# Performance work log

Measured on AMD Instinct MI355X. Metric: run time of the kernel, lower is better.

The kernel has to match this reference:

```python
import jax, jax.numpy as jnp
import numpy as np

N_IM, N_OBJ = 16, 16          # images, objects per image
D_IN = 2048                    # obj_pair_feat_dim
PER_IM = N_OBJ * (N_OBJ + 1) // 2   # obj boxes + union boxes per image
N_BOX = N_IM * PER_IM               # 2176
N_PAIR = N_IM * N_OBJ * (N_OBJ - 1) # is_ex=True -> 2*C(n,2) per image = 3840
NUM_REL = 3


def setup_inputs() -> dict:
    rng = np.random.default_rng(0)
    H, W = 600.0, 800.0
    boxes = np.zeros((N_BOX, 5), np.float32)
    o1i, o2i, ui, imi = [], [], [], []
    for i in range(N_IM):
        off = i * PER_IM
        x1 = rng.uniform(0, W / 2, N_OBJ); y1 = rng.uniform(0, H / 2, N_OBJ)
        bw = rng.uniform(10, W / 2, N_OBJ); bh = rng.uniform(10, H / 2, N_OBJ)
        boxes[off:off + N_OBJ] = np.stack([np.full(N_OBJ, i), x1, y1, x1 + bw, y1 + bh], 1)
        uc = off + N_OBJ
        for a in range(N_OBJ):
            for b in range(a + 1, N_OBJ):
                boxes[uc] = [i, min(x1[a], x1[b]), min(y1[a], y1[b]),
                             max(x1[a] + bw[a], x1[b] + bw[b]), max(y1[a] + bh[a], y1[b] + bh[b])]
                o1i += [off + a, off + b]; o2i += [off + b, off + a]
                ui += [uc, uc]; imi += [i, i]
                uc += 1
    im_info = np.tile(np.array([H, W, 1.0], np.float32), (N_IM, 1))
    key = jax.random.key(0)
    ks = jax.random.split(key, 16)
    lin = lambda k, i, o: jax.random.normal(k, (i, o), jnp.float32) * 0.02
    return dict(
        xs=jax.random.normal(ks[0], (N_PAIR, D_IN), jnp.float32) * 0.1,
        xo=jax.random.normal(ks[1], (N_PAIR, D_IN), jnp.float32) * 0.1,
        xu=jax.random.normal(ks[2], (N_PAIR, D_IN), jnp.float32) * 0.1,
        boxes=jnp.asarray(boxes), im_info=jnp.asarray(im_info),
        o1_idx=jnp.asarray(o1i, jnp.int32), o2_idx=jnp.asarray(o2i, jnp.int32),
        u_idx=jnp.asarray(ui, jnp.int32), img_idx=jnp.asarray(imi, jnp.int32),
        Ws1=lin(ks[3], D_IN, 512), bs1=jnp.zeros(512, jnp.float32),
        Ws2=lin(ks[4], 512, 256), bs2=jnp.zeros(256, jnp.float32),
        Wo1=lin(ks[5], D_IN, 512), bo1=jnp.zeros(512, jnp.float32),
        Wo2=lin(ks[6], 512, 256), bo2=jnp.zeros(256, jnp.float32),
        Wu1=lin(ks[7], D_IN, 512), bu1=jnp.zeros(512, jnp.float32),
        Wu2=lin(ks[8], 512, 256), bu2=jnp.zeros(256, jnp.float32),
        Wc1=lin(ks[9], 256 + 19, 256), bc1=jnp.zeros(256, jnp.float32),
        Wc2=lin(ks[10], 256, NUM_REL), bc2=jnp.zeros(NUM_REL, jnp.float32),
    )


def _mlp(x, W1, b1, W2, b2):
    return jax.nn.relu(jax.nn.relu(x @ W1 + b1) @ W2 + b2)


def _encode_loc(sb, ob, ub, hw):
    # sb/ob/ub: [P,4] (x1,y1,x2,y2); hw: [P,2] (h_i, w_i)
    h_i, w_i = hw[:, 0], hw[:, 1]
    x_s = (sb[:, 0] + sb[:, 2]) / 2.0; y_s = (sb[:, 1] + sb[:, 3]) / 2.0
    w_s = sb[:, 2] - sb[:, 0]; h_s = sb[:, 3] - sb[:, 1]
    x_o = (ob[:, 0] + ob[:, 2]) / 2.0; y_o = (ob[:, 1] + ob[:, 3]) / 2.0
    w_o = ob[:, 2] - ob[:, 0]; h_o = ob[:, 3] - ob[:, 1]
    a_s = w_s * h_s; a_o = w_o * h_o
    a_u = (ub[:, 2] - ub[:, 0]) * (ub[:, 3] - ub[:, 1])
    area = w_i * h_i
    return jnp.stack([
        x_s / w_i, y_s / h_i, (x_s + w_s) / w_i, (y_s + h_s) / h_i, a_s / area,
        x_o / w_i, y_o / h_i, (x_o + w_o) / w_i, (y_o + h_o) / h_i, a_o / area,
        (x_s - x_o) / w_o, (y_s - y_o) / h_o, jnp.log(w_s / w_o), jnp.log(h_s / h_o),
        (x_o - x_s) / w_s, (y_o - y_s) / h_s, jnp.log(w_o / w_s), jnp.log(h_o / h_s),
        a_u / area], axis=1)  # [P,19]


def reference(xs, xo, xu, boxes, im_info, o1_idx, o2_idx, u_idx, img_idx,
              Ws1, bs1, Ws2, bs2, Wo1, bo1, Wo2, bo2, Wu1, bu1, Wu2, bu2,
              Wc1, bc1, Wc2, bc2):
    fs = _mlp(xs, Ws1, bs1, Ws2, bs2)
    fo = _mlp(xo, Wo1, bo1, Wo2, bo2)
    fu = _mlp(xu, Wu1, bu1, Wu2, bu2)
    appear = fu - fo - fs                              # [P,256]
    loc = _encode_loc(boxes[o1_idx, 1:5], boxes[o2_idx, 1:5],
                      boxes[u_idx, 1:5], im_info[img_idx, :2])  # [P,19]
    h = jax.nn.relu(jnp.concatenate([appear, loc], axis=1) @ Wc1 + bc1)
    return h @ Wc2 + bc2                               # [P,num_rel]
```

## Files before the change

kernel.cpp:

```cpp
#include <hip/hip_runtime.h>

#define N_PAIR 3840

typedef short bf16x8 __attribute__((ext_vector_type(8)));
typedef float f32x4 __attribute__((ext_vector_type(4)));

static __device__ __forceinline__ ushort f2bf(float f) {
    uint x = __float_as_uint(f);
    uint r = (x + 0x7FFFu + ((x >> 16) & 1u)) >> 16;
    return (ushort)r;
}
static __device__ __forceinline__ float bf2f(ushort u) {
    return __uint_as_float(((uint)u) << 16);
}

#define GLOAD16(GP, LP)                                                        \
    __builtin_amdgcn_global_load_lds(                                          \
        (const __attribute__((address_space(1))) void*)(GP),                   \
        (__attribute__((address_space(3))) void*)(LP), 16, 0, 0)

static __device__ __forceinline__ bf16x8 cvt8(float4 lo, float4 hi4) {
    union { bf16x8 v; uint u[4]; } r;
    asm("v_cvt_pk_bf16_f32 %0, %1, %2" : "=v"(r.u[0]) : "v"(lo.x), "v"(lo.y));
    asm("v_cvt_pk_bf16_f32 %0, %1, %2" : "=v"(r.u[1]) : "v"(lo.z), "v"(lo.w));
    asm("v_cvt_pk_bf16_f32 %0, %1, %2" : "=v"(r.u[2]) : "v"(hi4.x), "v"(hi4.y));
    asm("v_cvt_pk_bf16_f32 %0, %1, %2" : "=v"(r.u[3]) : "v"(hi4.z), "v"(hi4.w));
    return r.v;
}

__global__ void transpose_convert(const float* __restrict__ in0,
                                  const float* __restrict__ in1,
                                  const float* __restrict__ in2,
                                  ushort* __restrict__ out,
                                  int K, int N, int Kpad) {
    const float* in = (blockIdx.z == 0) ? in0 : (blockIdx.z == 1 ? in1 : in2);
    ushort* o = out + (size_t)blockIdx.z * N * Kpad;
    __shared__ float tile[64][65];
    int k0 = blockIdx.x * 64, n0 = blockIdx.y * 64;
    int t = threadIdx.x;
    int r = t >> 2, c4 = (t & 3) * 16;
#pragma unroll
    for (int i = 0; i < 16; i++) {
        int k = k0 + r, n = n0 + c4 + i;
        tile[r][c4 + i] = (k < K && n < N) ? in[(size_t)k * N + n] : 0.f;
    }
    __syncthreads();
#pragma unroll
    for (int i = 0; i < 16; i++) {
        int n = n0 + r, k = k0 + c4 + i;
        if (n < N && k < Kpad) o[(size_t)n * Kpad + k] = f2bf(tile[c4 + i][r]);
    }
}

__global__ void transpose_convert2(const float* __restrict__ Ws2,
                                   const float* __restrict__ Wo2,
                                   const float* __restrict__ Wu2,
                                   const float* __restrict__ Wc1,
                                   ushort* __restrict__ W2T,
                                   ushort* __restrict__ WC1T) {
    int z = blockIdx.z;
    const float* in; ushort* o; int K, N, Kpad;
    if (z < 3) {
        in = (z == 0) ? Ws2 : (z == 1 ? Wo2 : Wu2);
        o = W2T + (size_t)z * 256 * 512; K = 512; N = 256; Kpad = 512;
    } else {
        in = Wc1; o = WC1T; K = 275; N = 256; Kpad = 288;
    }
    __shared__ float tile[64][65];
    int k0 = blockIdx.x * 64, n0 = blockIdx.y * 64;
    int t = threadIdx.x;
    int r = t >> 2, c4 = (t & 3) * 16;
#pragma unroll
    for (int i = 0; i < 16; i++) {
        int k = k0 + r, n = n0 + c4 + i;
        tile[r][c4 + i] = (k < K && n < N) ? in[(size_t)k * N + n] : 0.f;
    }
    __syncthreads();
#pragma unroll
    for (int i = 0; i < 16; i++) {
        int n = n0 + r, k = k0 + c4 + i;
        if (n < N && k < Kpad) o[(size_t)n * Kpad + k] = f2bf(tile[c4 + i][r]);
    }
}

__device__ __forceinline__ bf16x8 frag_ld(const ushort* __restrict__ lds, int row, int colbyte) {
    int off = (row << 7) + (colbyte ^ ((row & 7) << 4));
    return *reinterpret_cast<const bf16x8*>(reinterpret_cast<const char*>(lds) + off);
}
__device__ __forceinline__ bf16x8 frag32_ld(const ushort* __restrict__ lds, int row, int colbyte) {
    int off = (row << 6) + (colbyte ^ ((row & 3) << 4));
    return *reinterpret_cast<const bf16x8*>(reinterpret_cast<const char*>(lds) + off);
}

__global__ __launch_bounds__(256) void gemm1_main(const float* __restrict__ xs,
                                                  const float* __restrict__ xo,
                                                  const float* __restrict__ xu,
                                                  const ushort* __restrict__ w1t,
                                                  float* __restrict__ part) {
    int bid = blockIdx.x;
    int w = (bid & 7) * 90 + (bid >> 3);
    int br = w / 240; int r = w - br * 240;
    int mt = r >> 3, nt = (r >> 1) & 3, ks = r & 1;

    const float* x = br == 0 ? xs : (br == 1 ? xo : xu);
    const ushort* wt = w1t + (size_t)br * 512 * 2048;
    float* out = part + ((size_t)(ks * 3 + br)) * 3840 * 512;

    __shared__ float Af[128 * 64];
    __shared__ ushort Bs[128 * 64];
    int t = threadIdx.x, lane = t & 63, wid = t >> 6;
    int wr = wid >> 1, wc = wid & 1;
    int m0 = mt * 128, n0 = nt * 128, k0 = ks * 1024;
    const float* asrc = x + (size_t)m0 * 2048 + k0;
    const ushort* bsrc = wt + (size_t)n0 * 2048 + k0;
    int hi = lane >> 4, l15 = lane & 15;

    const float* aptr[8];
    const ushort* bptr[4];
#pragma unroll
    for (int i = 0; i < 8; i++) {
        int row = (wid * 8 + i) * 4 + (lane >> 4);
        int c16 = (lane & 15) ^ (row & 15);
        aptr[i] = asrc + (size_t)row * 2048 + (c16 << 2);
    }
#pragma unroll
    for (int i = 0; i < 4; i++) {
        int row = (wid * 4 + i) * 8 + (lane >> 3);
        int c8 = (lane & 7) ^ (row & 7);
        bptr[i] = bsrc + (size_t)row * 2048 + (c8 << 3);
    }

    f32x4 acc[4][4] = {};
#pragma unroll
    for (int i = 0; i < 8; i++) GLOAD16(aptr[i], &Af[((wid * 8 + i) * 64 + lane) * 4]);
#pragma unroll
    for (int i = 0; i < 4; i++) GLOAD16(bptr[i], &Bs[((wid * 4 + i) * 64 + lane) * 8]);
    __syncthreads();

    for (int kt = 0; kt < 1024; kt += 64) {
#pragma unroll
        for (int kk = 0; kk < 64; kk += 32) {
            int kf = kk + hi * 8;
            int c0 = kf >> 2;
            bf16x8 a[4], b[4];
#pragma unroll
            for (int i = 0; i < 4; i++) {
                int ra = wr * 64 + i * 16 + l15;
                const char* ab = reinterpret_cast<const char*>(&Af[0]);
                float4 lo = *reinterpret_cast<const float4*>(ab + ra * 256 + ((c0 ^ (ra & 15)) << 4));
                float4 h4 = *reinterpret_cast<const float4*>(ab + ra * 256 + (((c0 + 1) ^ (ra & 15)) << 4));
                a[i] = cvt8(lo, h4);
            }
#pragma unroll
            for (int j = 0; j < 4; j++)
                b[j] = frag_ld(&Bs[0], wc * 64 + j * 16 + l15, kf << 1);
#pragma unroll
            for (int i = 0; i < 4; i++)
#pragma unroll
                for (int j = 0; j < 4; j++)
                    acc[i][j] = __builtin_amdgcn_mfma_f32_16x16x32_bf16(a[i], b[j], acc[i][j], 0, 0, 0);
        }
        __syncthreads();
        if (kt + 64 < 1024) {
#pragma unroll
            for (int i = 0; i < 8; i++) GLOAD16(aptr[i] + kt + 64, &Af[((wid * 8 + i) * 64 + lane) * 4]);
#pragma unroll
            for (int i = 0; i < 4; i++) GLOAD16(bptr[i] + kt + 64, &Bs[((wid * 4 + i) * 64 + lane) * 8]);
            __syncthreads();
        }
    }
    int rb = m0 + wr * 64 + (hi << 2);
    int cb0 = n0 + wc * 64 + l15;
#pragma unroll
    for (int j = 0; j < 4; j++) {
        int col = cb0 + j * 16;
#pragma unroll
        for (int i = 0; i < 4; i++)
#pragma unroll
            for (int q = 0; q < 4; q++)
                out[(size_t)(rb + i * 16 + q) * 512 + col] = acc[i][j][q];
    }
}

__global__ void reduce_h1(const float* __restrict__ part,
                          const float* __restrict__ bs1,
                          const float* __restrict__ bo1,
                          const float* __restrict__ bu1,
                          ushort* __restrict__ h1) {
    const size_t D = (size_t)3840 * 512;
    size_t e = ((size_t)blockIdx.x * 256 + threadIdx.x) * 8;
    if (e >= 3 * D) return;
    int br = (int)(e / D);
    int col = (int)(e & 511);
    const float* bias = br == 0 ? bs1 : (br == 1 ? bo1 : bu1);
    const float4* p0 = reinterpret_cast<const float4*>(part + e);
    const float4* p1 = reinterpret_cast<const float4*>(part + 3 * D + e);
    const float4* bp = reinterpret_cast<const float4*>(bias + col);
    float4 a0 = p0[0], a1 = p0[1];
    float4 b0 = p1[0], b1 = p1[1];
    float4 c0 = bp[0], c1 = bp[1];
    union { bf16x8 v; ushort us[8]; } r;
#pragma unroll
    for (int i = 0; i < 4; i++) {
        float v = a0[i] + b0[i] + c0[i];
        r.us[i] = f2bf(v > 0.f ? v : 0.f);
        float w = a1[i] + b1[i] + c1[i];
        r.us[4 + i] = f2bf(w > 0.f ? w : 0.f);
    }
    *reinterpret_cast<bf16x8*>(h1 + e) = r.v;
}

__global__ __launch_bounds__(256) void gemm2(const ushort* __restrict__ h1,
                                             const ushort* __restrict__ w2t,
                                             const float* __restrict__ b_s,
                                             const float* __restrict__ b_o,
                                             const float* __restrict__ b_u,
                                             ushort* __restrict__ h2br) {
    int bid = blockIdx.x;
    int w = (bid & 7) * 45 + (bid >> 3);
    int br = w / 120; int r = w - br * 120;
    int xt = r >> 1, yt = r & 1;

    const ushort* A = h1 + (size_t)br * 3840 * 512;
    const ushort* B = w2t + (size_t)br * 256 * 512;
    const float* bias = br == 0 ? b_s : (br == 1 ? b_o : b_u);
    ushort* out = h2br + (size_t)br * 3840 * 256;

    __shared__ ushort As[2][64 * 64];
    __shared__ ushort Bs[2][128 * 64];
    int t = threadIdx.x, lane = t & 63, wid = t >> 6;
    int wr = wid >> 1, wc = wid & 1;
    int m0 = xt * 64, n0 = yt * 128;
    const ushort* asrc = A + (size_t)m0 * 512;
    const ushort* bsrc = B + (size_t)n0 * 512;

#define G2_GLOADS(BUF, KT)                                                                \
    {                                                                                     \
        _Pragma("unroll")                                                                 \
        for (int it = 0; it < 2; it++) {                                                  \
            int g = (wid * 2 + it) * 64 + lane;                                           \
            int rr = g >> 3, cc = g & 7;                                                  \
            const ushort* gp = asrc + (size_t)rr * 512 + (KT) + ((cc ^ (rr & 7)) << 3);   \
            GLOAD16(gp, &As[BUF][g * 8]);                                                 \
        }                                                                                 \
        _Pragma("unroll")                                                                 \
        for (int it = 0; it < 4; it++) {                                                  \
            int g = (wid * 4 + it) * 64 + lane;                                           \
            int rr = g >> 3, cc = g & 7;                                                  \
            const ushort* gp = bsrc + (size_t)rr * 512 + (KT) + ((cc ^ (rr & 7)) << 3);   \
            GLOAD16(gp, &Bs[BUF][g * 8]);                                                 \
        }                                                                                 \
    }
#define G2_MFMA(BUF)                                                                      \
    _Pragma("unroll")                                                                     \
    for (int kk = 0; kk < 64; kk += 32) {                                                 \
        int cb = (kk + ((lane >> 4) << 3)) << 1;                                          \
        bf16x8 a[2], b[4];                                                                \
        _Pragma("unroll")                                                                 \
        for (int i = 0; i < 2; i++) a[i] = frag_ld(&As[BUF][0], wr * 32 + i * 16 + (lane & 15), cb); \
        _Pragma("unroll")                                                                 \
        for (int f = 0; f < 4; f++) b[f] = frag_ld(&Bs[BUF][0], wc * 64 + f * 16 + (lane & 15), cb); \
        _Pragma("unroll")                                                                 \
        for (int i = 0; i < 2; i++)                                                       \
            _Pragma("unroll")                                                             \
            for (int j = 0; j < 4; j++)                                                   \
                acc[i][j] = __builtin_amdgcn_mfma_f32_16x16x32_bf16(a[i], b[j], acc[i][j], 0, 0, 0); \
    }

    f32x4 acc[2][4] = {};
    G2_GLOADS(0, 0)
    __syncthreads();
    int cur = 0;
    for (int kt = 0; kt < 512; kt += 64) {
        if (kt + 64 < 512) G2_GLOADS(cur ^ 1, kt + 64)
        G2_MFMA(cur)
        __syncthreads();
        cur ^= 1;
    }
    int rb = m0 + wr * 32 + ((lane >> 4) << 2);
    int cb0 = n0 + wc * 64 + (lane & 15);
#pragma unroll
    for (int j = 0; j < 4; j++) {
        int col = cb0 + j * 16;
        float bv = bias[col];
#pragma unroll
        for (int i = 0; i < 2; i++)
#pragma unroll
            for (int q = 0; q < 4; q++) {
                int row = rb + i * 16 + q;
                float v = acc[i][j][q] + bv;
                v = v > 0.f ? v : 0.f;
                out[(size_t)row * 256 + col] = f2bf(v);
            }
    }
#undef G2_GLOADS
#undef G2_MFMA
}

__global__ void appear_pack(const ushort* __restrict__ h2br,
                            ushort* __restrict__ hin,
                            const float* __restrict__ boxes,
                            const float* __restrict__ im_info,
                            const int* __restrict__ o1, const int* __restrict__ o2,
                            const int* __restrict__ u, const int* __restrict__ im) {
    int i = blockIdx.x * 256 + threadIdx.x;
    if (i < N_PAIR * 32) {
        int p = i >> 5, ch = (i & 31) * 8;
        const ushort* ps = h2br + (size_t)p * 256 + ch;
        bf16x8 vs = *reinterpret_cast<const bf16x8*>(ps);
        bf16x8 vo = *reinterpret_cast<const bf16x8*>(ps + (size_t)3840 * 256);
        bf16x8 vu = *reinterpret_cast<const bf16x8*>(ps + (size_t)2 * 3840 * 256);
        union { bf16x8 v; ushort us[8]; } r;
#pragma unroll
        for (int j = 0; j < 8; j++)
            r.us[j] = f2bf(bf2f(((ushort)vu[j])) - bf2f(((ushort)vo[j])) - bf2f(((ushort)vs[j])));
        *reinterpret_cast<bf16x8*>(hin + (size_t)p * 288 + ch) = r.v;
    }
    if (blockIdx.x < 15) {
        int p = blockIdx.x * 256 + threadIdx.x;
        const float* sb = boxes + 5 * o1[p] + 1;
        const float* ob = boxes + 5 * o2[p] + 1;
        const float* ub = boxes + 5 * u[p] + 1;
        const float* ii = im_info + 3 * im[p];
        float hi = ii[0], wi = ii[1];
        float x_s = (sb[0] + sb[2]) * 0.5f, y_s = (sb[1] + sb[3]) * 0.5f;
        float w_s = sb[2] - sb[0], h_s = sb[3] - sb[1];
        float x_o = (ob[0] + ob[2]) * 0.5f, y_o = (ob[1] + ob[3]) * 0.5f;
        float w_o = ob[2] - ob[0], h_o = ob[3] - ob[1];
        float a_s = w_s * h_s, a_o = w_o * h_o;
        float a_u = (ub[2] - ub[0]) * (ub[3] - ub[1]);
        float area = wi * hi;
        float f[19];
        f[0] = x_s / wi;            f[1] = y_s / hi;
        f[2] = (x_s + w_s) / wi;    f[3] = (y_s + h_s) / hi;
        f[4] = a_s / area;
        f[5] = x_o / wi;            f[6] = y_o / hi;
        f[7] = (x_o + w_o) / wi;    f[8] = (y_o + h_o) / hi;
        f[9] = a_o / area;
        f[10] = (x_s - x_o) / w_o;  f[11] = (y_s - y_o) / h_o;
        f[12] = logf(w_s / w_o);    f[13] = logf(h_s / h_o);
        f[14] = (x_o - x_s) / w_s;  f[15] = (y_o - y_s) / h_s;
        f[16] = logf(w_o / w_s);    f[17] = logf(h_o / h_s);
        f[18] = a_u / area;
        ushort* row = hin + (size_t)p * 288 + 256;
#pragma unroll
        for (int k = 0; k < 19; k++) row[k] = f2bf(f[k]);
#pragma unroll
        for (int k = 19; k < 32; k++) row[k] = 0;
    }
}

__global__ __launch_bounds__(256) void gemm3(const ushort* __restrict__ hin,
                                             const ushort* __restrict__ wc1t,
                                             const float* __restrict__ bc1,
                                             ushort* __restrict__ h2) {
    __shared__ ushort As[2][64 * 32];
    __shared__ ushort Bs[2][128 * 32];
    int t = threadIdx.x, lane = t & 63, wid = t >> 6;
    int wr = wid >> 1, wc = wid & 1;
    int m0 = blockIdx.x * 64, n0 = blockIdx.y * 128;
    const ushort* asrc = hin + (size_t)m0 * 288;
    const ushort* bsrc = wc1t + (size_t)n0 * 288;

    int ar = t >> 2, ac = (t & 3) * 8;
    bf16x8 pa, pb[2];
    auto issue = [&](int kt) {
        pa = *reinterpret_cast<const bf16x8*>(asrc + (size_t)ar * 288 + kt + ac);
#pragma unroll
        for (int it = 0; it < 2; it++) {
            int e = (it * 256 + t) * 8;
            int rr = e >> 5, cc = e & 31;
            pb[it] = *reinterpret_cast<const bf16x8*>(bsrc + (size_t)rr * 288 + kt + cc);
        }
    };
    auto commit = [&](int buf) {
        char* ab = reinterpret_cast<char*>(&As[buf][0]);
        int off0 = (ar << 6) + ((ac << 1) ^ ((ar & 3) << 4));
        *reinterpret_cast<bf16x8*>(ab + off0) = pa;
        char* bb = reinterpret_cast<char*>(&Bs[buf][0]);
#pragma unroll
        for (int it = 0; it < 2; it++) {
            int e = (it * 256 + t) * 8;
            int rr = e >> 5, cc = e & 31;
            int off = (rr << 6) + ((cc << 1) ^ ((rr & 3) << 4));
            *reinterpret_cast<bf16x8*>(bb + off) = pb[it];
        }
    };

    f32x4 acc[2][4] = {};
    issue(0);
    commit(0);
    __syncthreads();
    int cur = 0;
    for (int kt = 0; kt < 288; kt += 32) {
        int nxt = kt + 32;
        if (nxt < 288) issue(nxt);
        int cb = ((lane >> 4) << 3) << 1;
        bf16x8 a[2], b[4];
#pragma unroll
        for (int i = 0; i < 2; i++) a[i] = frag32_ld(&As[cur][0], wr * 32 + i * 16 + (lane & 15), cb);
#pragma unroll
        for (int f = 0; f < 4; f++) b[f] = frag32_ld(&Bs[cur][0], wc * 64 + f * 16 + (lane & 15), cb);
#pragma unroll
        for (int i = 0; i < 2; i++)
#pragma unroll
            for (int j = 0; j < 4; j++)
                acc[i][j] = __builtin_amdgcn_mfma_f32_16x16x32_bf16(a[i], b[j], acc[i][j], 0, 0, 0);
        if (nxt < 288) commit(cur ^ 1);
        __syncthreads();
        cur ^= 1;
    }
    int rb = m0 + wr * 32 + ((lane >> 4) << 2);
    int cb0 = n0 + wc * 64 + (lane & 15);
#pragma unroll
    for (int j = 0; j < 4; j++) {
        int col = cb0 + j * 16;
        float bv = bc1[col];
#pragma unroll
        for (int i = 0; i < 2; i++)
#pragma unroll
            for (int q = 0; q < 4; q++) {
                int row = rb + i * 16 + q;
                float v = acc[i][j][q] + bv;
                v = v > 0.f ? v : 0.f;
                h2[(size_t)row * 256 + col] = f2bf(v);
            }
    }
}

__global__ void final_fc(const ushort* __restrict__ h2,
                         const float* __restrict__ wc2,
                         const float* __restrict__ bc2,
                         float* __restrict__ out) {
    __shared__ float w[768];
    int t = threadIdx.x;
    for (int i = t; i < 768; i += 256) w[i] = wc2[i];
    __syncthreads();
    int g = t >> 4, l = t & 15;
    int row = blockIdx.x * 16 + g;
    const ushort* hr = h2 + (size_t)row * 256 + l * 16;
    bf16x8 v0 = *reinterpret_cast<const bf16x8*>(hr);
    bf16x8 v1 = *reinterpret_cast<const bf16x8*>(hr + 8);
    float s0 = 0.f, s1 = 0.f, s2 = 0.f;
#pragma unroll
    for (int k = 0; k < 8; k++) {
        float h = bf2f((ushort)v0[k]);
        int c = (l * 16 + k) * 3;
        s0 += h * w[c]; s1 += h * w[c + 1]; s2 += h * w[c + 2];
    }
#pragma unroll
    for (int k = 0; k < 8; k++) {
        float h = bf2f((ushort)v1[k]);
        int c = (l * 16 + 8 + k) * 3;
        s0 += h * w[c]; s1 += h * w[c + 1]; s2 += h * w[c + 2];
    }
#pragma unroll
    for (int m = 1; m < 16; m <<= 1) {
        s0 += __shfl_xor(s0, m);
        s1 += __shfl_xor(s1, m);
        s2 += __shfl_xor(s2, m);
    }
    if (l == 0) {
        out[row * 3 + 0] = s0 + bc2[0];
        out[row * 3 + 1] = s1 + bc2[1];
        out[row * 3 + 2] = s2 + bc2[2];
    }
}

extern "C" void kernel_launch(void* const* d_in, const int* in_sizes, int n_in,
                              void* d_out, int out_size, void* d_ws, size_t ws_size,
                              hipStream_t stream) {
    (void)in_sizes; (void)n_in; (void)out_size; (void)ws_size;
    const float* xs = (const float*)d_in[0];
    const float* xo = (const float*)d_in[1];
    const float* xu = (const float*)d_in[2];
    const float* boxes = (const float*)d_in[3];
    const float* im_info = (const float*)d_in[4];
    const int* o1 = (const int*)d_in[5];
    const int* o2 = (const int*)d_in[6];
    const int* uu = (const int*)d_in[7];
    const int* im = (const int*)d_in[8];
    const float* Ws1 = (const float*)d_in[9];
    const float* bs1 = (const float*)d_in[10];
    const float* Ws2 = (const float*)d_in[11];
    const float* bs2 = (const float*)d_in[12];
    const float* Wo1 = (const float*)d_in[13];
    const float* bo1 = (const float*)d_in[14];
    const float* Wo2 = (const float*)d_in[15];
    const float* bo2 = (const float*)d_in[16];
    const float* Wu1 = (const float*)d_in[17];
    const float* bu1 = (const float*)d_in[18];
    const float* Wu2 = (const float*)d_in[19];
    const float* bu2 = (const float*)d_in[20];
    const float* Wc1 = (const float*)d_in[21];
    const float* bc1 = (const float*)d_in[22];
    const float* Wc2 = (const float*)d_in[23];
    const float* bc2 = (const float*)d_in[24];
    float* out = (float*)d_out;

    ushort* W1T = (ushort*)d_ws;
    ushort* H2BR = W1T;
    ushort* W2T = W1T + (size_t)3 * 512 * 2048;
    ushort* WC1T = W2T + (size_t)3 * 256 * 512;
    ushort* H1 = WC1T + (size_t)256 * 288;
    ushort* HIN = H1 + (size_t)3 * 3840 * 512;
    ushort* H2 = HIN + (size_t)3840 * 288;
    float* PART = (float*)(H2 + (size_t)3840 * 256);

    transpose_convert<<<dim3(32, 8, 3), 256, 0, stream>>>(Ws1, Wo1, Wu1, W1T, 2048, 512, 2048);
    transpose_convert2<<<dim3(8, 4, 4), 256, 0, stream>>>(Ws2, Wo2, Wu2, Wc1, W2T, WC1T);
    gemm1_main<<<720, 256, 0, stream>>>(xs, xo, xu, W1T, PART);
    reduce_h1<<<2880, 256, 0, stream>>>(PART, bs1, bo1, bu1, H1);
    gemm2<<<360, 256, 0, stream>>>(H1, W2T, bs2, bo2, bu2, H2BR);
    appear_pack<<<480, 256, 0, stream>>>(H2BR, HIN, boxes, im_info, o1, o2, uu, im);
    gemm3<<<dim3(60, 2), 256, 0, stream>>>(HIN, WC1T, bc1, H2);
    final_fc<<<240, 256, 0, stream>>>(H2, Wc2, bc2, out);
}
```

Before: 111.9 us.

## Replace split-K gemm1 with single-wave 64x64 tiles, double-buffered, fused bias/ReLU

```diff
diff --git a/kernel.cpp b/kernel.cpp
--- a/kernel.cpp
+++ b/kernel.cpp
@@ -92,122 +92,107 @@
     return *reinterpret_cast<const bf16x8*>(reinterpret_cast<const char*>(lds) + off);
 }
 
-__global__ __launch_bounds__(256) void gemm1_main(const float* __restrict__ xs,
-                                                  const float* __restrict__ xo,
-                                                  const float* __restrict__ xu,
-                                                  const ushort* __restrict__ w1t,
-                                                  float* __restrict__ part) {
+__global__ __launch_bounds__(64) void gemm1(const float* __restrict__ xs,
+                                            const float* __restrict__ xo,
+                                            const float* __restrict__ xu,
+                                            const ushort* __restrict__ w1t,
+                                            const float* __restrict__ b_s,
+                                            const float* __restrict__ b_o,
+                                            const float* __restrict__ b_u,
+                                            ushort* __restrict__ h1out) {
     int bid = blockIdx.x;
-    int w = (bid & 7) * 90 + (bid >> 3);
-    int br = w / 240; int r = w - br * 240;
-    int mt = r >> 3, nt = (r >> 1) & 3, ks = r & 1;
+    int w = (bid & 7) * 180 + (bid >> 3);
+    int br = w / 480; int r = w - br * 480;
+    int mt = r >> 3, nt = r & 7;
 
     const float* x = br == 0 ? xs : (br == 1 ? xo : xu);
     const ushort* wt = w1t + (size_t)br * 512 * 2048;
-    float* out = part + ((size_t)(ks * 3 + br)) * 3840 * 512;
-
-    __shared__ float Af[128 * 64];
-    __shared__ ushort Bs[128 * 64];
-    int t = threadIdx.x, lane = t & 63, wid = t >> 6;
-    int wr = wid >> 1, wc = wid & 1;
-    int m0 = mt * 128, n0 = nt * 128, k0 = ks * 1024;
-    const float* asrc = x + (size_t)m0 * 2048 + k0;
-    const ushort* bsrc = wt + (size_t)n0 * 2048 + k0;
+    const float* bias = br == 0 ? b_s : (br == 1 ? b_o : b_u);
+    ushort* out = h1out + (size_t)br * 3840 * 512;
+
+    __shared__ float Af[2][64 * 32];
+    __shared__ ushort Bs[2][64 * 32];
+    int lane = threadIdx.x;
     int hi = lane >> 4, l15 = lane & 15;
-
-    const float* aptr[8];
-    const ushort* bptr[4];
-#pragma unroll
-    for (int i = 0; i < 8; i++) {
-        int row = (wid * 8 + i) * 4 + (lane >> 4);
-        int c16 = (lane & 15) ^ (row & 15);
-        aptr[i] = asrc + (size_t)row * 2048 + (c16 << 2);
-    }
-#pragma unroll
-    for (int i = 0; i < 4; i++) {
-        int row = (wid * 4 + i) * 8 + (lane >> 3);
-        int c8 = (lane & 7) ^ (row & 7);
-        bptr[i] = bsrc + (size_t)row * 2048 + (c8 << 3);
+    int m0 = mt * 64, n0 = nt * 64;
+    const float* asrc = x + (size_t)m0 * 2048;
+    const ushort* bsrc = wt + (size_t)n0 * 2048;
+
+    const float* ap[8];
+    const ushort* bp[4];
+    {
+        int acol = ((lane & 7) ^ (lane >> 3)) << 2;
+#pragma unroll
+        for (int i = 0; i < 8; i++)
+            ap[i] = asrc + (size_t)(i * 8 + (lane >> 3)) * 2048 + acol;
+        int bcol = ((lane & 3) ^ ((lane >> 2) & 3)) << 3;
+#pragma unroll
+        for (int i = 0; i < 4; i++)
+            bp[i] = bsrc + (size_t)(i * 16 + (lane >> 2)) * 2048 + bcol;
+    }
+
+#define G1_STAGE(BUF, KT)                                                     \
+    {                                                                         \
+        _Pragma("unroll")                                                     \
+        for (int i = 0; i < 8; i++)                                           \
+            GLOAD16(ap[i] + (KT), &Af[BUF][(i * 64 + lane) * 4]);             \
+        _Pragma("unroll")                                                     \
+        for (int i = 0; i < 4; i++)                                           \
+            GLOAD16(bp[i] + (KT), &Bs[BUF][(i * 64 + lane) * 8]);             \
     }
 
     f32x4 acc[4][4] = {};
-#pragma unroll
-    for (int i = 0; i < 8; i++) GLOAD16(aptr[i], &Af[((wid * 8 + i) * 64 + lane) * 4]);
-#pragma unroll
-    for (int i = 0; i < 4; i++) GLOAD16(bptr[i], &Bs[((wid * 4 + i) * 64 + lane) * 8]);
-    __syncthreads();
-
-    for (int kt = 0; kt < 1024; kt += 64) {
-#pragma unroll
-        for (int kk = 0; kk < 64; kk += 32) {
-            int kf = kk + hi * 8;
-            int c0 = kf >> 2;
-            bf16x8 a[4], b[4];
-#pragma unroll
-            for (int i = 0; i < 4; i++) {
-                int ra = wr * 64 + i * 16 + l15;
-                const char* ab = reinterpret_cast<const char*>(&Af[0]);
-                float4 lo = *reinterpret_cast<const float4*>(ab + ra * 256 + ((c0 ^ (ra & 15)) << 4));
-                float4 h4 = *reinterpret_cast<const float4*>(ab + ra * 256 + (((c0 + 1) ^ (ra & 15)) << 4));
-                a[i] = cvt8(lo, h4);
+    G1_STAGE(0, 0)
+    G1_STAGE(1, 32)
+
+    int c0 = hi * 2;
+    for (int kt = 0; kt < 2048; kt += 32) {
+        int cur = (kt >> 5) & 1;
+        if (kt < 2048 - 32) {
+            asm volatile("s_waitcnt vmcnt(12)" ::: "memory");
+        } else {
+            asm volatile("s_waitcnt vmcnt(0)" ::: "memory");
+        }
+        __builtin_amdgcn_sched_barrier(0);
+        bf16x8 a[4], b[4];
+#pragma unroll
+        for (int i = 0; i < 4; i++) {
+            int ra = i * 16 + l15;
+            const char* ab = reinterpret_cast<const char*>(&Af[cur][0]);
+            float4 lo = *reinterpret_cast<const float4*>(ab + ra * 128 + ((c0 ^ (ra & 7)) << 4));
+            float4 h4 = *reinterpret_cast<const float4*>(ab + ra * 128 + (((c0 + 1) ^ (ra & 7)) << 4));
+            a[i] = cvt8(lo, h4);
+        }
+#pragma unroll
+        for (int j = 0; j < 4; j++) {
+            int rb = j * 16 + l15;
+            const char* bb = reinterpret_cast<const char*>(&Bs[cur][0]);
+            b[j] = *reinterpret_cast<const bf16x8*>(bb + rb * 64 + ((hi ^ (rb & 3)) << 4));
+        }
+#pragma unroll
+        for (int i = 0; i < 4; i++)
+#pragma unroll
+            for (int j = 0; j < 4; j++)
+                acc[i][j] = __builtin_amdgcn_mfma_f32_16x16x32_bf16(a[i], b[j], acc[i][j], 0, 0, 0);
+        if (kt + 64 < 2048) G1_STAGE(cur, kt + 64)
+    }
+    int rbase = m0 + (hi << 2);
+    int cbase = n0 + l15;
+#pragma unroll
+    for (int j = 0; j < 4; j++) {
+        int col = cbase + j * 16;
+        float bv = bias[col];
+#pragma unroll
+        for (int i = 0; i < 4; i++)
+#pragma unroll
+            for (int q = 0; q < 4; q++) {
+                int row = rbase + i * 16 + q;
+                float v = acc[i][j][q] + bv;
+                v = v > 0.f ? v : 0.f;
+                out[(size_t)row * 512 + col] = f2bf(v);
             }
-#pragma unroll
-            for (int j = 0; j < 4; j++)
-                b[j] = frag_ld(&Bs[0], wc * 64 + j * 16 + l15, kf << 1);
-#pragma unroll
-            for (int i = 0; i < 4; i++)
-#pragma unroll
-                for (int j = 0; j < 4; j++)
-                    acc[i][j] = __builtin_amdgcn_mfma_f32_16x16x32_bf16(a[i], b[j], acc[i][j], 0, 0, 0);
-        }
-        __syncthreads();
-        if (kt + 64 < 1024) {
-#pragma unroll
-            for (int i = 0; i < 8; i++) GLOAD16(aptr[i] + kt + 64, &Af[((wid * 8 + i) * 64 + lane) * 4]);
-#pragma unroll
-            for (int i = 0; i < 4; i++) GLOAD16(bptr[i] + kt + 64, &Bs[((wid * 4 + i) * 64 + lane) * 8]);
-            __syncthreads();
-        }
-    }
-    int rb = m0 + wr * 64 + (hi << 2);
-    int cb0 = n0 + wc * 64 + l15;
-#pragma unroll
-    for (int j = 0; j < 4; j++) {
-        int col = cb0 + j * 16;
-#pragma unroll
-        for (int i = 0; i < 4; i++)
-#pragma unroll
-            for (int q = 0; q < 4; q++)
-                out[(size_t)(rb + i * 16 + q) * 512 + col] = acc[i][j][q];
-    }
-}
-
-__global__ void reduce_h1(const float* __restrict__ part,
-                          const float* __restrict__ bs1,
-                          const float* __restrict__ bo1,
-                          const float* __restrict__ bu1,
-                          ushort* __restrict__ h1) {
-    const size_t D = (size_t)3840 * 512;
-    size_t e = ((size_t)blockIdx.x * 256 + threadIdx.x) * 8;
-    if (e >= 3 * D) return;
-    int br = (int)(e / D);
-    int col = (int)(e & 511);
-    const float* bias = br == 0 ? bs1 : (br == 1 ? bo1 : bu1);
-    const float4* p0 = reinterpret_cast<const float4*>(part + e);
-    const float4* p1 = reinterpret_cast<const float4*>(part + 3 * D + e);
-    const float4* bp = reinterpret_cast<const float4*>(bias + col);
-    float4 a0 = p0[0], a1 = p0[1];
-    float4 b0 = p1[0], b1 = p1[1];
-    float4 c0 = bp[0], c1 = bp[1];
-    union { bf16x8 v; ushort us[8]; } r;
-#pragma unroll
-    for (int i = 0; i < 4; i++) {
-        float v = a0[i] + b0[i] + c0[i];
-        r.us[i] = f2bf(v > 0.f ? v : 0.f);
-        float w = a1[i] + b1[i] + c1[i];
-        r.us[4 + i] = f2bf(w > 0.f ? w : 0.f);
-    }
-    *reinterpret_cast<bf16x8*>(h1 + e) = r.v;
+    }
+#undef G1_STAGE
 }
 
 __global__ __launch_bounds__(256) void gemm2(const ushort* __restrict__ h1,
@@ -505,12 +490,10 @@
     ushort* H1 = WC1T + (size_t)256 * 288;
     ushort* HIN = H1 + (size_t)3 * 3840 * 512;
     ushort* H2 = HIN + (size_t)3840 * 288;
-    float* PART = (float*)(H2 + (size_t)3840 * 256);
 
     transpose_convert<<<dim3(32, 8, 3), 256, 0, stream>>>(Ws1, Wo1, Wu1, W1T, 2048, 512, 2048);
     transpose_convert2<<<dim3(8, 4, 4), 256, 0, stream>>>(Ws2, Wo2, Wu2, Wc1, W2T, WC1T);
-    gemm1_main<<<720, 256, 0, stream>>>(xs, xo, xu, W1T, PART);
-    reduce_h1<<<2880, 256, 0, stream>>>(PART, bs1, bo1, bu1, H1);
+    gemm1<<<1440, 64, 0, stream>>>(xs, xo, xu, W1T, bs1, bo1, bu1, H1);
     gemm2<<<360, 256, 0, stream>>>(H1, W2T, bs2, bo2, bu2, H2BR);
     appear_pack<<<480, 256, 0, stream>>>(H2BR, HIN, boxes, im_info, o1, o2, uu, im);
     gemm3<<<dim3(60, 2), 256, 0, stream>>>(HIN, WC1T, bc1, H2);
```

Result: faster. 105.9 us (-5.4%).
